# Performance work log

Measured on AMD Instinct MI355X. Metric: run time of the kernel, lower is better.

The kernel has to match this reference:

```python
import jax, jax.numpy as jnp
import numpy as np

HEADS = 6
WL = 8  # window_length; N = WL*WL = 64 tokens per window


def _relative_position_index(wl):
    coords = jnp.stack(jnp.meshgrid(jnp.arange(wl), jnp.arange(wl), indexing='ij'))  # [2, wl, wl]
    cf = coords.reshape(2, -1)                                # [2, N]
    rel = cf[:, :, None] - cf[:, None, :]                     # [2, N, N]
    rel = rel.transpose(1, 2, 0) + (wl - 1)                   # shift to >= 0
    return rel[..., 0] * (2 * wl - 1) + rel[..., 1]           # [N, N] in [0, (2wl-1)^2)


def setup_inputs() -> dict:
    key = jax.random.key(0)
    ks = jax.random.split(key, 5)
    nW, N, C = 4096, WL * WL, 192
    x = jax.random.normal(ks[0], (nW, N, C), dtype=jnp.float32)
    mask = jnp.zeros((nW, N, N), dtype=jnp.float32)
    qkv_w = jax.random.normal(ks[1], (3 * C, C), dtype=jnp.float32) * 0.02
    qkv_b = jnp.zeros((3 * C,), dtype=jnp.float32)
    proj_w = jax.random.normal(ks[2], (C, C), dtype=jnp.float32) * 0.02
    proj_b = jnp.zeros((C,), dtype=jnp.float32)
    bias_table = jax.random.normal(ks[3], ((2 * WL - 1) ** 2, HEADS), dtype=jnp.float32) * 0.02
    return {"x": x, "mask": mask, "qkv_w": qkv_w, "qkv_b": qkv_b,
            "proj_w": proj_w, "proj_b": proj_b, "bias_table": bias_table}


def reference(x, mask, qkv_w, qkv_b, proj_w, proj_b, bias_table):
    nW, N, C = x.shape
    dh = C // HEADS
    scale = dh ** -0.5
    # qkv projection: [nW, N, 3C] -> q,k,v each [nW, heads, N, dh]
    qkv = (jnp.einsum('wnc,oc->wno', x, qkv_w) + qkv_b).reshape(nW, N, 3, HEADS, dh)
    q, k, v = (qkv[:, :, i].transpose(0, 2, 1, 3) for i in range(3))
    # windowed attention logits + gathered relative position bias + mask
    attn = jnp.einsum('whnd,whmd->whnm', q * scale, k)        # [nW, heads, N, N]
    rpi = _relative_position_index(WL)                        # [N, N] int
    rel_bias = bias_table[rpi].transpose(2, 0, 1)             # [heads, N, N]
    attn = attn + rel_bias[None] + mask[:, None]              # broadcast over heads
    attn = jax.nn.softmax(attn, axis=-1)
    out = jnp.einsum('whnm,whmd->whnd', attn, v)              # [nW, heads, N, dh]
    out = out.transpose(0, 2, 1, 3).reshape(nW, N, C)
    return jnp.einsum('wnc,oc->wno', out, proj_w) + proj_b
```

## Files before the change

### kernel.cpp

```cpp
#include <hip/hip_runtime.h>
#include <hip/hip_bf16.h>
#include <cstddef>

#define NTOK   64
#define CDIM   192
#define HEADS  6
#define NTHR   768
#define SCALE  0.17677669529663687f

#define WQ_ELEMS (3*CDIM*CDIM)
#define WP_ELEMS (CDIM*CDIM)

#define OFF_MASK 24576
#define OFF_K    41984
#define OFF_V    66560
#define LDS_BYTES 91136

typedef __attribute__((ext_vector_type(8))) short bf16x8;
typedef __attribute__((ext_vector_type(4))) short bf16x4;
typedef __attribute__((ext_vector_type(4))) float f32x4;
typedef __attribute__((ext_vector_type(4))) unsigned int u32x4;

static __device__ __forceinline__ unsigned short f2b(float f) {
    __hip_bfloat16 h = __float2bfloat16(f);
    return __builtin_bit_cast(unsigned short, h);
}
static __device__ __forceinline__ char* swz384(char* base, int row, int b) {
    return base + ((row * 384 + b) ^ ((row & 7) << 4));
}
static __device__ __forceinline__ char* swz64(char* base, int row, int b) {
    return base + row * 64 + (b ^ (((row >> 1) & 3) << 4));
}
static __device__ __forceinline__ char* swz128(char* base, int row, int b) {
    return base + ((row * 128 + b) ^ ((row & 7) << 4));
}

static __device__ __forceinline__ uint2 packq4(f32x4 v, float4 b) {
    unsigned short e0 = f2b(v[0] + b.x), e1 = f2b(v[1] + b.y);
    unsigned short e2 = f2b(v[2] + b.z), e3 = f2b(v[3] + b.w);
    uint2 q; q.x = (unsigned)e0 | ((unsigned)e1 << 16);
             q.y = (unsigned)e2 | ((unsigned)e3 << 16);
    return q;
}
static __device__ __forceinline__ uint2 packq0(f32x4 v) {
    unsigned short e0 = f2b(v[0]), e1 = f2b(v[1]);
    unsigned short e2 = f2b(v[2]), e3 = f2b(v[3]);
    uint2 q; q.x = (unsigned)e0 | ((unsigned)e1 << 16);
             q.y = (unsigned)e2 | ((unsigned)e3 << 16);
    return q;
}

static __device__ __forceinline__ void p8(uint2 a, uint2 b, int lo, int hi,
                                          uint2& oa, uint2& ob) {
    int sA = lo + ((hi & 1) << 5);
    int sB = sA + 16;
    uint2 Aa, Ab, Ba, Bb;
    Aa.x = (unsigned)__shfl((int)a.x, sA); Aa.y = (unsigned)__shfl((int)a.y, sA);
    Ab.x = (unsigned)__shfl((int)b.x, sA); Ab.y = (unsigned)__shfl((int)b.y, sA);
    Ba.x = (unsigned)__shfl((int)a.x, sB); Ba.y = (unsigned)__shfl((int)a.y, sB);
    Bb.x = (unsigned)__shfl((int)b.x, sB); Bb.y = (unsigned)__shfl((int)b.y, sB);
    oa = (hi < 2) ? Aa : Ab;
    ob = (hi < 2) ? Ba : Bb;
}
static __device__ __forceinline__ bf16x8 mkfrag(uint2 oa, uint2 ob) {
    u32x4 u; u[0] = oa.x; u[1] = oa.y; u[2] = ob.x; u[3] = ob.y;
    return __builtin_bit_cast(bf16x8, u);
}

__global__ __launch_bounds__(256)
void prep_weights(const float* __restrict__ qkv_w, const float* __restrict__ proj_w,
                  unsigned short* __restrict__ wq, unsigned short* __restrict__ wp)
{
    int i = blockIdx.x * 256 + threadIdx.x;
    if (i < WQ_ELEMS) {
        float v = qkv_w[i];
        if (i < CDIM * CDIM) v *= SCALE;
        wq[i] = f2b(v);
    }
    if (i < WP_ELEMS) wp[i] = f2b(proj_w[i]);
}

__global__ __launch_bounds__(NTHR, 3)
void win_attn(const float* __restrict__ x,
              const float* __restrict__ mask,
              const unsigned short* __restrict__ wq,
              const float* __restrict__ qkv_b,
              const unsigned short* __restrict__ wp,
              const float* __restrict__ proj_b,
              const float* __restrict__ bias_table,
              float* __restrict__ out)
{
    extern __shared__ char smem[];
    char*  XA    = smem;
    float* maskL = (float*)(smem + OFF_MASK);

    const int t    = threadIdx.x;
    const int w    = blockIdx.x;
    const int wv   = t >> 6;
    const int h    = wv >> 1;
    const int half = wv & 1;
    const int l    = t & 63;
    const int lo   = l & 15;
    const int hi   = l >> 4;

    char* Kh = smem + OFF_K + h * 4096;
    char* Vh = smem + OFF_V + h * 4096;

    const float* xw = x + (size_t)w * (NTOK * CDIM);
    #pragma unroll
    for (int it = 0; it < 2; ++it) {
        int c  = t + it * NTHR;
        int n  = c / 24;
        int cb = (c % 24) * 8;
        float4 v0 = *(const float4*)(xw + c * 8);
        float4 v1 = *(const float4*)(xw + c * 8 + 4);
        bf16x8 p;
        p[0] = (short)f2b(v0.x); p[1] = (short)f2b(v0.y);
        p[2] = (short)f2b(v0.z); p[3] = (short)f2b(v0.w);
        p[4] = (short)f2b(v1.x); p[5] = (short)f2b(v1.y);
        p[6] = (short)f2b(v1.z); p[7] = (short)f2b(v1.w);
        *(bf16x8*)swz384(XA, n, cb * 2) = p;
    }
    const float* mw = mask + (size_t)w * (NTOK * NTOK);
    #pragma unroll
    for (int it = 0; it < 2; ++it) {
        int c = t + it * NTHR;
        if (c < 1024) {
            float4 v = *(const float4*)(mw + c * 4);
            *(float4*)(maskL + (c >> 4) * 68 + (c & 15) * 4) = v;
        }
    }
    __syncthreads();

    const int tq = 2 * h, tk = 12 + 2 * h, tv = 24 + 2 * h;
    f32x4 aq[2][2] = {}, ak[2][2] = {}, av[2][2] = {};
    for (int ks = 0; ks < 6; ++ks) {
        bf16x8 xf[2];
        #pragma unroll
        for (int ntl = 0; ntl < 2; ++ntl)
            xf[ntl] = *(const bf16x8*)swz384(XA, (half * 2 + ntl) * 16 + lo,
                                             (ks * 32 + hi * 8) * 2);
        bf16x8 wqf[2], wkf[2], wvf[2];
        #pragma unroll
        for (int j = 0; j < 2; ++j) {
            wqf[j] = *(const bf16x8*)(const void*)(wq + ((tq + j) * 16 + lo) * CDIM + ks * 32 + hi * 8);
            wkf[j] = *(const bf16x8*)(const void*)(wq + ((tk + j) * 16 + lo) * CDIM + ks * 32 + hi * 8);
            wvf[j] = *(const bf16x8*)(const void*)(wq + ((tv + j) * 16 + lo) * CDIM + ks * 32 + hi * 8);
        }
        #pragma unroll
        for (int j = 0; j < 2; ++j)
            #pragma unroll
            for (int ntl = 0; ntl < 2; ++ntl) {
                aq[j][ntl] = __builtin_amdgcn_mfma_f32_16x16x32_bf16(wqf[j], xf[ntl], aq[j][ntl], 0, 0, 0);
                ak[j][ntl] = __builtin_amdgcn_mfma_f32_16x16x32_bf16(wkf[j], xf[ntl], ak[j][ntl], 0, 0, 0);
                av[ntl][j] = __builtin_amdgcn_mfma_f32_16x16x32_bf16(xf[ntl], wvf[j], av[ntl][j], 0, 0, 0);
            }
    }

    bf16x8 Qf[2];
    {
        float4 bq0 = *(const float4*)(qkv_b + tq * 16 + hi * 4);
        float4 bq1 = *(const float4*)(qkv_b + (tq + 1) * 16 + hi * 4);
        bq0.x *= SCALE; bq0.y *= SCALE; bq0.z *= SCALE; bq0.w *= SCALE;
        bq1.x *= SCALE; bq1.y *= SCALE; bq1.z *= SCALE; bq1.w *= SCALE;
        #pragma unroll
        for (int ntl = 0; ntl < 2; ++ntl) {
            uint2 oa, ob;
            p8(packq4(aq[0][ntl], bq0), packq4(aq[1][ntl], bq1), lo, hi, oa, ob);
            Qf[ntl] = mkfrag(oa, ob);
        }
    }
    #pragma unroll
    for (int j = 0; j < 2; ++j) {
        float4 bk = *(const float4*)(qkv_b + (tk + j) * 16 + hi * 4);
        float bkr[4] = {bk.x, bk.y, bk.z, bk.w};
        #pragma unroll
        for (int mtl = 0; mtl < 2; ++mtl) {
            int m = (half * 2 + mtl) * 16 + lo;
            bf16x4 pk;
            #pragma unroll
            for (int r = 0; r < 4; ++r) pk[r] = (short)f2b(ak[j][mtl][r] + bkr[r]);
            *(bf16x4*)swz64(Kh, m, j * 32 + hi * 8) = pk;
        }
    }
    #pragma unroll
    for (int mtl = 0; mtl < 2; ++mtl)
        #pragma unroll
        for (int j = 0; j < 2; ++j) {
            float bv = qkv_b[(tv + j) * 16 + lo];
            bf16x4 pv;
            #pragma unroll
            for (int r = 0; r < 4; ++r) pv[r] = (short)f2b(av[mtl][j][r] + bv);
            *(bf16x4*)swz128(Vh, j * 16 + lo, ((half * 2 + mtl) * 16 + hi * 4) * 2) = pv;
        }
    __syncthreads();

    bf16x8 Kf[4];
    #pragma unroll
    for (int mt = 0; mt < 4; ++mt)
        Kf[mt] = *(const bf16x8*)swz64(Kh, mt * 16 + lo, hi * 16);

    f32x4 cs[4][2];
    #pragma unroll
    for (int ntl = 0; ntl < 2; ++ntl) {
        int n  = (half * 2 + ntl) * 16 + lo;
        int i1 = n >> 3, j1 = n & 7;
        #pragma unroll
        for (int mt = 0; mt < 4; ++mt) {
            float4 mv = *(const float4*)(maskL + n * 68 + mt * 16 + hi * 4);
            float mvr[4] = {mv.x, mv.y, mv.z, mv.w};
            #pragma unroll
            for (int r = 0; r < 4; ++r) {
                int m  = mt * 16 + hi * 4 + r;
                int i2 = m >> 3, j2 = m & 7;
                cs[mt][ntl][r] = bias_table[((i1 - i2 + 7) * 15 + (j1 - j2 + 7)) * HEADS + h]
                               + mvr[r];
            }
        }
    }
    #pragma unroll
    for (int mt = 0; mt < 4; ++mt)
        #pragma unroll
        for (int ntl = 0; ntl < 2; ++ntl)
            cs[mt][ntl] = __builtin_amdgcn_mfma_f32_16x16x32_bf16(Kf[mt], Qf[ntl], cs[mt][ntl], 0, 0, 0);

    bf16x8 Pf[2][2];
    #pragma unroll
    for (int ntl = 0; ntl < 2; ++ntl) {
        float mx = cs[0][ntl][0];
        #pragma unroll
        for (int mt = 0; mt < 4; ++mt)
            #pragma unroll
            for (int r = 0; r < 4; ++r) mx = fmaxf(mx, cs[mt][ntl][r]);
        mx = fmaxf(mx, __shfl_xor(mx, 16));
        mx = fmaxf(mx, __shfl_xor(mx, 32));
        float s = 0.f;
        #pragma unroll
        for (int mt = 0; mt < 4; ++mt)
            #pragma unroll
            for (int r = 0; r < 4; ++r) {
                float e = __expf(cs[mt][ntl][r] - mx);
                cs[mt][ntl][r] = e;
                s += e;
            }
        s += __shfl_xor(s, 16);
        s += __shfl_xor(s, 32);
        float iv = 1.0f / s;
        #pragma unroll
        for (int mt = 0; mt < 4; ++mt)
            #pragma unroll
            for (int r = 0; r < 4; ++r) cs[mt][ntl][r] *= iv;
        uint2 oa, ob;
        p8(packq0(cs[0][ntl]), packq0(cs[1][ntl]), lo, hi, oa, ob);
        Pf[0][ntl] = mkfrag(oa, ob);
        p8(packq0(cs[2][ntl]), packq0(cs[3][ntl]), lo, hi, oa, ob);
        Pf[1][ntl] = mkfrag(oa, ob);
    }

    f32x4 co[2][2] = {};
    #pragma unroll
    for (int ks = 0; ks < 2; ++ks) {
        bf16x8 vb[2];
        #pragma unroll
        for (int dt = 0; dt < 2; ++dt)
            vb[dt] = *(const bf16x8*)swz128(Vh, dt * 16 + lo, (ks * 32 + hi * 8) * 2);
        #pragma unroll
        for (int ntl = 0; ntl < 2; ++ntl)
            #pragma unroll
            for (int dt = 0; dt < 2; ++dt)
                co[ntl][dt] = __builtin_amdgcn_mfma_f32_16x16x32_bf16(Pf[ks][ntl], vb[dt], co[ntl][dt], 0, 0, 0);
    }
    #pragma unroll
    for (int ntl = 0; ntl < 2; ++ntl)
        #pragma unroll
        for (int dt = 0; dt < 2; ++dt)
            #pragma unroll
            for (int r = 0; r < 4; ++r) {
                int n = (half * 2 + ntl) * 16 + hi * 4 + r;
                *(unsigned short*)swz384(XA, n, (h * 32 + dt * 16 + lo) * 2) =
                    f2b(co[ntl][dt][r]);
            }
    __syncthreads();

    f32x4 ac[4] = {};
    const int o2 = wv * 16 + lo;
    for (int ks = 0; ks < 6; ++ks) {
        bf16x8 bb = *(const bf16x8*)(const void*)(wp + o2 * CDIM + ks * 32 + hi * 8);
        #pragma unroll
        for (int nt = 0; nt < 4; ++nt) {
            bf16x8 aa = *(const bf16x8*)swz384(XA, nt * 16 + lo, (ks * 32 + hi * 8) * 2);
            ac[nt] = __builtin_amdgcn_mfma_f32_16x16x32_bf16(aa, bb, ac[nt], 0, 0, 0);
        }
    }
    float* outW = out + (size_t)w * (NTOK * CDIM);
    float pb = proj_b[o2];
    #pragma unroll
    for (int nt = 0; nt < 4; ++nt)
        #pragma unroll
        for (int r = 0; r < 4; ++r) {
            int n = nt * 16 + hi * 4 + r;
            outW[n * CDIM + o2] = ac[nt][r] + pb;
        }
}

extern "C" void kernel_launch(void* const* d_in, const int* in_sizes, int n_in,
                              void* d_out, int out_size, void* d_ws, size_t ws_size,
                              hipStream_t stream) {
    const float* x          = (const float*)d_in[0];
    const float* mask       = (const float*)d_in[1];
    const float* qkv_w      = (const float*)d_in[2];
    const float* qkv_b      = (const float*)d_in[3];
    const float* proj_w     = (const float*)d_in[4];
    const float* proj_b     = (const float*)d_in[5];
    const float* bias_table = (const float*)d_in[6];
    float* out = (float*)d_out;

    unsigned short* wq = (unsigned short*)d_ws;
    unsigned short* wp = wq + WQ_ELEMS;

    const int nW = in_sizes[0] / (NTOK * CDIM);

    prep_weights<<<dim3((WQ_ELEMS + 255) / 256), dim3(256), 0, stream>>>(qkv_w, proj_w, wq, wp);

    hipFuncSetAttribute(reinterpret_cast<const void*>(win_attn),
                        hipFuncAttributeMaxDynamicSharedMemorySize, LDS_BYTES);
    win_attn<<<dim3(nW), dim3(NTHR), LDS_BYTES, stream>>>(x, mask, wq, qkv_b, wp,
                                                          proj_b, bias_table, out);
}
```

Before: 390.9 us.

## Precompute dense relative bias and read mask from global to cut LDS

A prep kernel now expands the relative position bias table into a dense per-head [heads,N,N] array in workspace. The attention kernel then loads the bias with vector reads instead of per-element gathers with index arithmetic. The mask is no longer staged in LDS and is read straight from global memory in the logit init, so the LDS footprint shrinks. Launch bounds are raised so more blocks can be resident per CU. The cost is extra global traffic for the bias, possible register pressure from the higher occupancy target, and a fallback template path for when the workspace is too small.

After: 555.5 us. +42.1%, slower.

```diff
diff --git a/kernel.cpp b/kernel.cpp
--- a/kernel.cpp
+++ b/kernel.cpp
@@ -10,11 +10,13 @@
 
 #define WQ_ELEMS (3*CDIM*CDIM)
 #define WP_ELEMS (CDIM*CDIM)
-
-#define OFF_MASK 24576
-#define OFF_K    41984
-#define OFF_V    66560
-#define LDS_BYTES 91136
+#define RELB_ELEMS (HEADS*NTOK*NTOK)
+#define WS_RELB_OFF ((WQ_ELEMS+WP_ELEMS)*2)
+#define WS_NEED (WS_RELB_OFF + RELB_ELEMS*4)
+
+#define OFF_K    24576
+#define OFF_V    49152
+#define LDS_BYTES 73728
 
 typedef __attribute__((ext_vector_type(8))) short bf16x8;
 typedef __attribute__((ext_vector_type(4))) short bf16x4;
@@ -69,7 +71,9 @@
 
 __global__ __launch_bounds__(256)
 void prep_weights(const float* __restrict__ qkv_w, const float* __restrict__ proj_w,
-                  unsigned short* __restrict__ wq, unsigned short* __restrict__ wp)
+                  const float* __restrict__ bias_table,
+                  unsigned short* __restrict__ wq, unsigned short* __restrict__ wp,
+                  float* __restrict__ relb, int fill_relb)
 {
     int i = blockIdx.x * 256 + threadIdx.x;
     if (i < WQ_ELEMS) {
@@ -78,9 +82,17 @@
         wq[i] = f2b(v);
     }
     if (i < WP_ELEMS) wp[i] = f2b(proj_w[i]);
-}
-
-__global__ __launch_bounds__(NTHR, 3)
+    if (fill_relb && i < RELB_ELEMS) {
+        int h = i >> 12;
+        int rem = i & 4095;
+        int n = rem >> 6, m = rem & 63;
+        int i1 = n >> 3, j1 = n & 7, i2 = m >> 3, j2 = m & 7;
+        relb[i] = bias_table[((i1 - i2 + 7) * 15 + (j1 - j2 + 7)) * HEADS + h];
+    }
+}
+
+template <bool USE_RELB>
+__global__ __launch_bounds__(NTHR, 6)
 void win_attn(const float* __restrict__ x,
               const float* __restrict__ mask,
               const unsigned short* __restrict__ wq,
@@ -88,11 +100,11 @@
               const unsigned short* __restrict__ wp,
               const float* __restrict__ proj_b,
               const float* __restrict__ bias_table,
+              const float* __restrict__ relb,
               float* __restrict__ out)
 {
     extern __shared__ char smem[];
-    char*  XA    = smem;
-    float* maskL = (float*)(smem + OFF_MASK);
+    char* XA = smem;
 
     const int t    = threadIdx.x;
     const int w    = blockIdx.x;
@@ -121,15 +133,6 @@
         p[6] = (short)f2b(v1.z); p[7] = (short)f2b(v1.w);
         *(bf16x8*)swz384(XA, n, cb * 2) = p;
     }
-    const float* mw = mask + (size_t)w * (NTOK * NTOK);
-    #pragma unroll
-    for (int it = 0; it < 2; ++it) {
-        int c = t + it * NTHR;
-        if (c < 1024) {
-            float4 v = *(const float4*)(mw + c * 4);
-            *(float4*)(maskL + (c >> 4) * 68 + (c & 15) * 4) = v;
-        }
-    }
     __syncthreads();
 
     const int tq = 2 * h, tk = 12 + 2 * h, tv = 24 + 2 * h;
@@ -200,21 +203,31 @@
     for (int mt = 0; mt < 4; ++mt)
         Kf[mt] = *(const bf16x8*)swz64(Kh, mt * 16 + lo, hi * 16);
 
+    const float* mw = mask + (size_t)w * (NTOK * NTOK);
+    const float* rb = relb + h * (NTOK * NTOK);
     f32x4 cs[4][2];
     #pragma unroll
     for (int ntl = 0; ntl < 2; ++ntl) {
         int n  = (half * 2 + ntl) * 16 + lo;
-        int i1 = n >> 3, j1 = n & 7;
         #pragma unroll
         for (int mt = 0; mt < 4; ++mt) {
-            float4 mv = *(const float4*)(maskL + n * 68 + mt * 16 + hi * 4);
-            float mvr[4] = {mv.x, mv.y, mv.z, mv.w};
-            #pragma unroll
-            for (int r = 0; r < 4; ++r) {
-                int m  = mt * 16 + hi * 4 + r;
-                int i2 = m >> 3, j2 = m & 7;
-                cs[mt][ntl][r] = bias_table[((i1 - i2 + 7) * 15 + (j1 - j2 + 7)) * HEADS + h]
-                               + mvr[r];
+            float4 mv = *(const float4*)(mw + n * 64 + mt * 16 + hi * 4);
+            if constexpr (USE_RELB) {
+                float4 bv = *(const float4*)(rb + n * 64 + mt * 16 + hi * 4);
+                cs[mt][ntl][0] = mv.x + bv.x;
+                cs[mt][ntl][1] = mv.y + bv.y;
+                cs[mt][ntl][2] = mv.z + bv.z;
+                cs[mt][ntl][3] = mv.w + bv.w;
+            } else {
+                int i1 = n >> 3, j1 = n & 7;
+                float mvr[4] = {mv.x, mv.y, mv.z, mv.w};
+                #pragma unroll
+                for (int r = 0; r < 4; ++r) {
+                    int m  = mt * 16 + hi * 4 + r;
+                    int i2 = m >> 3, j2 = m & 7;
+                    cs[mt][ntl][r] = bias_table[((i1 - i2 + 7) * 15 + (j1 - j2 + 7)) * HEADS + h]
+                                   + mvr[r];
+                }
             }
         }
     }
@@ -317,13 +330,23 @@
 
     unsigned short* wq = (unsigned short*)d_ws;
     unsigned short* wp = wq + WQ_ELEMS;
+    float* relb = (float*)((char*)d_ws + WS_RELB_OFF);
 
     const int nW = in_sizes[0] / (NTOK * CDIM);
-
-    prep_weights<<<dim3((WQ_ELEMS + 255) / 256), dim3(256), 0, stream>>>(qkv_w, proj_w, wq, wp);
-
-    hipFuncSetAttribute(reinterpret_cast<const void*>(win_attn),
-                        hipFuncAttributeMaxDynamicSharedMemorySize, LDS_BYTES);
-    win_attn<<<dim3(nW), dim3(NTHR), LDS_BYTES, stream>>>(x, mask, wq, qkv_b, wp,
-                                                          proj_b, bias_table, out);
-}
+    const int use_relb = (ws_size >= (size_t)WS_NEED) ? 1 : 0;
+
+    prep_weights<<<dim3((WQ_ELEMS + 255) / 256), dim3(256), 0, stream>>>(
+        qkv_w, proj_w, bias_table, wq, wp, relb, use_relb);
+
+    if (use_relb) {
+        hipFuncSetAttribute(reinterpret_cast<const void*>(win_attn<true>),
+                            hipFuncAttributeMaxDynamicSharedMemorySize, LDS_BYTES);
+        win_attn<true><<<dim3(nW), dim3(NTHR), LDS_BYTES, stream>>>(
+            x, mask, wq, qkv_b, wp, proj_b, bias_table, relb, out);
+    } else {
+        hipFuncSetAttribute(reinterpret_cast<const void*>(win_attn<false>),
+                            hipFuncAttributeMaxDynamicSharedMemorySize, LDS_BYTES);
+        win_attn<false><<<dim3(nW), dim3(NTHR), LDS_BYTES, stream>>>(
+            x, mask, wq, qkv_b, wp, proj_b, bias_table, relb, out);
+    }
+}
```
